# Kernel optimization log

Measured on AMD Instinct MI355X. Metric: run time of the kernel, lower is better.

Reference implementation:

```python
import jax, jax.numpy as jnp
import numpy as np

N = 50000      # nodes
E = 800000     # edges
F_IN = 146
D = 256        # repr_len
H = 512        # GENConv hidden (expansion=2)
L = 25         # res blocks
EPS_MSG = 1e-7 # GENConv message eps
T = 0.01       # softmax aggregation temperature


def setup_inputs() -> dict:
    key = jax.random.key(0)
    ks = jax.random.split(key, 8)
    s = lambda k, shape, scale=0.05: jax.random.normal(k, shape, jnp.float32) * scale
    return dict(
        x=jax.random.uniform(ks[0], (N, F_IN), jnp.float32),
        edge_index=jax.random.randint(ks[1], (2, E), 0, N, jnp.int32),
        enc_W=s(ks[2], (F_IN, D)), enc_b=jnp.zeros((D,), jnp.float32),
        conv_W1=s(ks[3], (L, D, H)), conv_b1=jnp.zeros((L, H), jnp.float32),
        conv_ln_g=jnp.ones((L, H), jnp.float32), conv_ln_b=jnp.zeros((L, H), jnp.float32),
        conv_W2=s(ks[4], (L, H, D)), conv_b2=jnp.zeros((L, D), jnp.float32),
        res_ln_g=jnp.ones((L, D), jnp.float32), res_ln_b=jnp.zeros((L, D), jnp.float32),
        fc1_W=s(ks[5], (D, D // 2)), fc1_b=jnp.zeros((D // 2,), jnp.float32),
        out_W=s(ks[6], (D // 2, 1)), out_b=jnp.zeros((1,), jnp.float32),
    )


def layer_norm(x, g, b, eps=1e-5):
    mu = x.mean(-1, keepdims=True)
    var = ((x - mu) ** 2).mean(-1, keepdims=True)
    return (x - mu) * jax.lax.rsqrt(var + eps) * g + b


def genconv(x, src, dst, W1, b1, g1, bb1, W2, b2):
    # message: relu(x_j) + eps  (no edge_attr)
    msg = jax.nn.relu(x[src]) + EPS_MSG                    # [E, D]
    logit = msg * T
    m = jax.ops.segment_max(logit, dst, num_segments=N)    # per-dst, per-feature max
    m = jnp.where(jnp.isfinite(m), m, 0.0)                 # isolated nodes -> 0
    num = jnp.exp(logit - m[dst])
    den = jax.ops.segment_sum(num, dst, num_segments=N)
    alpha = num / (den[dst] + 1e-16)
    agg = jax.ops.segment_sum(alpha * msg, dst, num_segments=N)  # [N, D]
    h = agg + x                                            # root residual inside GENConv
    h = jax.nn.relu(layer_norm(h @ W1 + b1, g1, bb1))      # MLP: Lin->LN->ReLU->Lin
    return h @ W2 + b2


def reference(x, edge_index, enc_W, enc_b, conv_W1, conv_b1, conv_ln_g, conv_ln_b,
              conv_W2, conv_b2, res_ln_g, res_ln_b, fc1_W, fc1_b, out_W, out_b):
    src, dst = edge_index[0], edge_index[1]
    x = x.at[:, 121:].set(x[:, 121:] / 100.0 - 0.5)
    h = x @ enc_W + enc_b
    # layer 0: conv only
    h = genconv(h, src, dst, conv_W1[0], conv_b1[0], conv_ln_g[0], conv_ln_b[0],
                conv_W2[0], conv_b2[0])

    # layers 1..24: res+ block  (dropout=0.1 is identity in eval mode)
    def step(h, p):
        W1, b1, g1, bb1, W2, b2, rg, rb = p
        z = jax.nn.relu(layer_norm(h, rg, rb))
        z = genconv(z, src, dst, W1, b1, g1, bb1, W2, b2)
        return h + z, None

    params = (conv_W1[1:], conv_b1[1:], conv_ln_g[1:], conv_ln_b[1:],
              conv_W2[1:], conv_b2[1:], res_ln_g[1:], res_ln_b[1:])
    h, _ = jax.lax.scan(step, h, params)

    # final: layers[0].act(layers[0].norm(x))
    h = jax.nn.relu(layer_norm(h, res_ln_g[0], res_ln_b[0]))
    h = jax.nn.relu(h @ fc1_W + fc1_b)
    return h @ out_W + out_b
```

## Files before the change

kernel.cpp:

```cpp
#include <hip/hip_runtime.h>

#define NN 50000
#define NE 800000
#define FIN 146
#define DD 256
#define HHD 512
#define NL 25
#define MT 196
#define MT2 391
#define SCAN_NB 49

#define SWZ(r) (((r) >> 1) & 3)

typedef _Float16 h8 __attribute__((ext_vector_type(8)));
typedef float f32x4 __attribute__((ext_vector_type(4)));
typedef unsigned short us8 __attribute__((ext_vector_type(8)));
typedef _Float16 hf4 __attribute__((ext_vector_type(4)));

__device__ __forceinline__ float wsum(float v) {
#pragma unroll
  for (int off = 32; off > 0; off >>= 1) v += __shfl_xor(v, off, 64);
  return v;
}

__device__ __forceinline__ unsigned short f16b(float x) {
  _Float16 h = (_Float16)x;
  return __builtin_bit_cast(unsigned short, h);
}
__device__ __forceinline__ float f16f(unsigned short b) {
  return (float)__builtin_bit_cast(_Float16, b);
}

__device__ __forceinline__ void gl_lds16(const void* g, void* l) {
  __builtin_amdgcn_global_load_lds(
      (const __attribute__((address_space(1))) unsigned int*)g,
      (__attribute__((address_space(3))) unsigned int*)l, 16, 0, 0);
}

__global__ void count_k(const int* __restrict__ ei, int* __restrict__ deg) {
  int e = blockIdx.x * 256 + threadIdx.x;
  if (e < NE) atomicAdd(&deg[ei[NE + e]], 1);
}

__global__ __launch_bounds__(1024) void scan1_k(const int* __restrict__ deg,
                                                int* __restrict__ rp,
                                                int* __restrict__ bsum) {
  __shared__ int buf[1024];
  int tid = threadIdx.x, blk = blockIdx.x;
  int i = blk * 1024 + tid;
  buf[tid] = (i < NN) ? deg[i] : 0;
  __syncthreads();
#pragma unroll
  for (int off = 1; off < 1024; off <<= 1) {
    int t = (tid >= off) ? buf[tid - off] : 0;
    __syncthreads();
    buf[tid] += t;
    __syncthreads();
  }
  if (i < NN) rp[i + 1] = buf[tid];
  if (tid == 1023) bsum[blk] = buf[1023];
}

__global__ void scan2_k(int* __restrict__ bsum) {
  int tid = threadIdx.x;
  int v = (tid < SCAN_NB) ? bsum[tid] : 0;
#pragma unroll
  for (int off = 1; off < 64; off <<= 1) {
    int t = __shfl_up(v, off, 64);
    if (tid >= off) v += t;
  }
  if (tid < SCAN_NB) bsum[tid] = v;
}

__global__ __launch_bounds__(1024) void scan3_k(const int* __restrict__ bsum,
                                                int* __restrict__ rp,
                                                int* __restrict__ deg) {
  int i = blockIdx.x * 1024 + threadIdx.x;
  if (i < NN) {
    int blk = i >> 10;
    if (blk > 0) rp[i + 1] += bsum[blk - 1];
    deg[i] = 0;
  }
  if (i == 0) rp[0] = 0;
}

__global__ void fill_k(const int* __restrict__ ei, const int* __restrict__ rp,
                       int* __restrict__ deg, int* __restrict__ col) {
  int e = blockIdx.x * 256 + threadIdx.x;
  if (e < NE) {
    int d = ei[NE + e];
    int pos = rp[d] + atomicAdd(&deg[d], 1);
    col[pos] = ei[e];
  }
}

__global__ __launch_bounds__(256) void wconv_k(const float* __restrict__ cW1,
                                               const float* __restrict__ cW2,
                                               const float* __restrict__ fcW,
                                               const float* __restrict__ encW,
                                               unsigned short* __restrict__ wbuf,
                                               unsigned short* __restrict__ fc1t,
                                               unsigned short* __restrict__ encT) {
  int z = blockIdx.z;
  const float* W;
  unsigned short* oh;
  int Ksrc, Kpad, N;
  if (z < 50) {
    int l = z >> 1, which = z & 1;
    if (which == 0) { W = cW1 + (size_t)l * 131072; Ksrc = 256; N = 512; oh = wbuf + (size_t)l * 524288; }
    else            { W = cW2 + (size_t)l * 131072; Ksrc = 512; N = 256; oh = wbuf + (size_t)l * 524288 + 262144; }
    Kpad = Ksrc;
  } else if (z == 50) {
    W = fcW; Ksrc = 256; Kpad = 256; N = 128; oh = fc1t;
  } else {
    W = encW; Ksrc = FIN; Kpad = 160; N = 256; oh = encT;
  }
  if ((int)blockIdx.x >= (Kpad >> 5) || (int)blockIdx.y >= (N >> 5)) return;
  __shared__ float tile[32][33];
  int tx = threadIdx.x, ty = threadIdx.y;
  int k0 = blockIdx.x * 32, n0 = blockIdx.y * 32;
#pragma unroll
  for (int i = 0; i < 4; ++i) {
    int r = ty + i * 8;
    int k = k0 + r;
    tile[r][tx] = (k < Ksrc) ? W[(size_t)k * N + n0 + tx] : 0.f;
  }
  __syncthreads();
#pragma unroll
  for (int i = 0; i < 4; ++i) {
    int r = ty + i * 8;
    float v = tile[tx][r];
    oh[(size_t)(n0 + r) * Kpad + k0 + tx] = f16b(v);
  }
}

__global__ __launch_bounds__(256) void agg16_k(const hf4* __restrict__ z16,
                                               const int* __restrict__ rp,
                                               const int* __restrict__ col,
                                               unsigned short* __restrict__ hh16) {
  int node = blockIdx.x * 4 + (threadIdx.x >> 6);
  int lane = threadIdx.x & 63;
  if (node >= NN) return;
  int beg = rp[node], end = rp[node + 1];
  float4 s = make_float4(0.f, 0.f, 0.f, 0.f);
  float4 v = make_float4(0.f, 0.f, 0.f, 0.f);
  int j = beg;
  for (; j + 1 < end; j += 2) {
    int sn0 = col[j], sn1 = col[j + 1];
    hf4 a = z16[(size_t)sn0 * 64 + lane];
    hf4 c = z16[(size_t)sn1 * 64 + lane];
    float m0 = fmaxf((float)a[0], 0.f) + 1e-7f;
    float m1 = fmaxf((float)a[1], 0.f) + 1e-7f;
    float m2 = fmaxf((float)a[2], 0.f) + 1e-7f;
    float m3 = fmaxf((float)a[3], 0.f) + 1e-7f;
    float e0 = __expf(m0 * 0.01f), e1 = __expf(m1 * 0.01f);
    float e2 = __expf(m2 * 0.01f), e3 = __expf(m3 * 0.01f);
    s.x += e0; s.y += e1; s.z += e2; s.w += e3;
    v.x = fmaf(e0, m0, v.x); v.y = fmaf(e1, m1, v.y);
    v.z = fmaf(e2, m2, v.z); v.w = fmaf(e3, m3, v.w);
    float n0 = fmaxf((float)c[0], 0.f) + 1e-7f;
    float n1 = fmaxf((float)c[1], 0.f) + 1e-7f;
    float n2 = fmaxf((float)c[2], 0.f) + 1e-7f;
    float n3 = fmaxf((float)c[3], 0.f) + 1e-7f;
    float f0 = __expf(n0 * 0.01f), f1 = __expf(n1 * 0.01f);
    float f2 = __expf(n2 * 0.01f), f3 = __expf(n3 * 0.01f);
    s.x += f0; s.y += f1; s.z += f2; s.w += f3;
    v.x = fmaf(f0, n0, v.x); v.y = fmaf(f1, n1, v.y);
    v.z = fmaf(f2, n2, v.z); v.w = fmaf(f3, n3, v.w);
  }
  if (j < end) {
    int sn = col[j];
    hf4 a = z16[(size_t)sn * 64 + lane];
    float m0 = fmaxf((float)a[0], 0.f) + 1e-7f;
    float m1 = fmaxf((float)a[1], 0.f) + 1e-7f;
    float m2 = fmaxf((float)a[2], 0.f) + 1e-7f;
    float m3 = fmaxf((float)a[3], 0.f) + 1e-7f;
    float e0 = __expf(m0 * 0.01f), e1 = __expf(m1 * 0.01f);
    float e2 = __expf(m2 * 0.01f), e3 = __expf(m3 * 0.01f);
    s.x += e0; s.y += e1; s.z += e2; s.w += e3;
    v.x = fmaf(e0, m0, v.x); v.y = fmaf(e1, m1, v.y);
    v.z = fmaf(e2, m2, v.z); v.w = fmaf(e3, m3, v.w);
  }
  hf4 ow = z16[(size_t)node * 64 + lane];
  float o0 = v.x / (s.x + 1e-16f) + (float)ow[0];
  float o1 = v.y / (s.y + 1e-16f) + (float)ow[1];
  float o2 = v.z / (s.z + 1e-16f) + (float)ow[2];
  float o3 = v.w / (s.w + 1e-16f) + (float)ow[3];
  size_t idx = (size_t)node * DD + lane * 4;
  *(ushort4*)&hh16[idx] = make_ushort4(f16b(o0), f16b(o1), f16b(o2), f16b(o3));
}

template <int AMODE, int ACC, int RELU, int PSUM, int C16, int Z16>
__global__ __launch_bounds__(512, 3) void mgemm_k(
    const float* __restrict__ Af, const unsigned short* __restrict__ A16,
    const unsigned short* __restrict__ BTh,
    const float* __restrict__ bias, float* __restrict__ C, int M, int K, int N,
    int mtiles, int lgnb,
    const float2* __restrict__ stats,
    const float* __restrict__ lng, const float* __restrict__ lnbeta,
    float2* __restrict__ psum_out, unsigned short* __restrict__ z16out) {
  __shared__ __align__(16) unsigned short Ash[2][8192], Bsh[2][4096];
  int tid = threadIdx.x;
  int bi = blockIdx.x;
  int ppx = (mtiles + 7) >> 3;
  int slot = bi >> 3;
  int panel = (bi & 7) * ppx + (slot >> lgnb);
  if (panel >= mtiles) return;
  int nblk = slot & ((1 << lgnb) - 1);
  int bm0 = panel * 256, bn0 = nblk * 128;
  int lane = tid & 63, wv = tid >> 6;
  int wr = (wv >> 1) * 64, wc = (wv & 1) * 64;
  int lr = lane & 15, lc = lane >> 4;
  f32x4 acc[4][4];
  f32x4 zf = {0.f, 0.f, 0.f, 0.f};
#pragma unroll
  for (int mi = 0; mi < 4; ++mi)
#pragma unroll
    for (int ni = 0; ni < 4; ++ni) acc[mi][ni] = zf;

  int sr = tid >> 1, hf = tid & 1;
  int arow = bm0 + sr;

  float mu = 0.f, rstd = 1.f;
  if constexpr (AMODE == 3) {
    if (arow < M) {
      float2 st = stats[arow];
      mu = st.x; rstd = st.y;
    }
  }

  auto stageB = [&](int buf, int k0) {
    int r = tid >> 2, cp = tid & 3;
    int c = cp ^ SWZ(r);
    gl_lds16(BTh + (size_t)(bn0 + r) * K + k0 + c * 8, &Bsh[buf][wv * 512]);
  };
  auto stageA = [&](int buf, int k0) {
    if constexpr (AMODE == 0) {
#pragma unroll
      for (int j = 0; j < 2; ++j) {
        int idx = wv * 128 + j * 64 + lane;
        int r = idx >> 2, cp = idx & 3;
        int c = cp ^ SWZ(r);
        int row = bm0 + r;
        if (row >= M) row = M - 1;
        gl_lds16(A16 + (size_t)row * K + k0 + c * 8, &Ash[buf][wv * 1024 + j * 512]);
      }
    } else {
      float v[16];
      if (arow < M) {
        if constexpr (AMODE == 2) {
          const float* xp = Af + (size_t)arow * FIN;
#pragma unroll
          for (int j = 0; j < 16; ++j) {
            int kk = k0 + hf * 16 + j;
            float t = (kk < FIN) ? xp[kk] : 0.f;
            if (kk >= 121 && kk < FIN) t = t * 0.01f - 0.5f;
            v[j] = t;
          }
        } else {
          const float* ap = Af + (size_t)arow * K + k0 + hf * 16;
          *(float4*)&v[0] = *(const float4*)(ap);
          *(float4*)&v[4] = *(const float4*)(ap + 4);
          *(float4*)&v[8] = *(const float4*)(ap + 8);
          *(float4*)&v[12] = *(const float4*)(ap + 12);
          const float* gp = lng + k0 + hf * 16;
          const float* bp = lnbeta + k0 + hf * 16;
#pragma unroll
          for (int j = 0; j < 16; ++j)
            v[j] = fmaxf(0.f, (v[j] - mu) * rstd * gp[j] + bp[j]);
        }
      } else {
#pragma unroll
        for (int j = 0; j < 16; ++j) v[j] = 0.f;
      }
      unsigned short hi[16];
#pragma unroll
      for (int j = 0; j < 16; ++j) hi[j] = f16b(v[j]);
      int c0 = hf * 2;
      *(us8*)&Ash[buf][sr * 32 + ((c0 ^ SWZ(sr)) * 8)] = *(us8*)&hi[0];
      *(us8*)&Ash[buf][sr * 32 + (((c0 + 1) ^ SWZ(sr)) * 8)] = *(us8*)&hi[8];
    }
  };

  int nt = K / 32;
  stageA(0, 0);
  stageB(0, 0);
  __syncthreads();
  for (int t = 0; t < nt; ++t) {
    int cur = t & 1;
    h8 a[4], bh[4];
#pragma unroll
    for (int mi = 0; mi < 4; ++mi) {
      int r = wr + mi * 16 + lr;
      a[mi] = *(const h8*)&Ash[cur][r * 32 + ((lc ^ SWZ(r)) * 8)];
    }
#pragma unroll
    for (int ni = 0; ni < 4; ++ni) {
      int n = wc + ni * 16 + lr;
      bh[ni] = *(const h8*)&Bsh[cur][n * 32 + ((lc ^ SWZ(n)) * 8)];
    }
    if (t + 1 < nt) {
      stageA(cur ^ 1, (t + 1) * 32);
      stageB(cur ^ 1, (t + 1) * 32);
    }
    __builtin_amdgcn_s_setprio(1);
#pragma unroll
    for (int mi = 0; mi < 4; ++mi)
#pragma unroll
      for (int ni = 0; ni < 4; ++ni)
        acc[mi][ni] = __builtin_amdgcn_mfma_f32_16x16x32_f16(a[mi], bh[ni], acc[mi][ni], 0, 0, 0);
    __builtin_amdgcn_s_setprio(0);
    __syncthreads();
  }
  float sloc[16], qloc[16];
  if constexpr (PSUM) {
#pragma unroll
    for (int i = 0; i < 16; ++i) { sloc[i] = 0.f; qloc[i] = 0.f; }
  }
#pragma unroll
  for (int ni = 0; ni < 4; ++ni) {
    int colg = bn0 + wc + ni * 16 + lr;
    float bia = bias[colg];
#pragma unroll
    for (int mi = 0; mi < 4; ++mi) {
#pragma unroll
      for (int r = 0; r < 4; ++r) {
        int row = bm0 + wr + mi * 16 + lc * 4 + r;
        if (row < M) {
          float vv = acc[mi][ni][r] + bia;
          if (ACC) vv += C[(size_t)row * N + colg];
          if (RELU) vv = fmaxf(vv, 0.f);
          if constexpr (C16) {
            ((unsigned short*)C)[(size_t)row * N + colg] = f16b(vv);
          } else {
            C[(size_t)row * N + colg] = vv;
          }
          if constexpr (Z16) {
            z16out[(size_t)row * N + colg] = f16b(vv);
          }
          if constexpr (PSUM) {
            sloc[mi * 4 + r] += vv;
            qloc[mi * 4 + r] = fmaf(vv, vv, qloc[mi * 4 + r]);
          }
        }
      }
    }
  }
  if constexpr (PSUM) {
#pragma unroll
    for (int i = 0; i < 16; ++i) {
      float s = sloc[i], q = qloc[i];
#pragma unroll
      for (int off = 1; off < 16; off <<= 1) {
        s += __shfl_xor(s, off, 64);
        q += __shfl_xor(q, off, 64);
      }
      sloc[i] = s; qloc[i] = q;
    }
    __syncthreads();
    float2* lps = (float2*)&Ash[0][0];
    if (wv & 1) {
      if (lr == 0) {
#pragma unroll
        for (int mi = 0; mi < 4; ++mi)
#pragma unroll
          for (int r = 0; r < 4; ++r)
            lps[(wv >> 1) * 64 + mi * 16 + lc * 4 + r] =
                make_float2(sloc[mi * 4 + r], qloc[mi * 4 + r]);
      }
    }
    __syncthreads();
    if (!(wv & 1)) {
      if (lr == 0) {
#pragma unroll
        for (int mi = 0; mi < 4; ++mi)
#pragma unroll
          for (int r = 0; r < 4; ++r) {
            int rl = mi * 16 + lc * 4 + r;
            float2 o = lps[(wv >> 1) * 64 + rl];
            int row = bm0 + wr + rl;
            if (row < M)
              psum_out[(size_t)row * 4 + nblk] =
                  make_float2(sloc[mi * 4 + r] + o.x, qloc[mi * 4 + r] + o.y);
          }
      }
    }
  }
}

template <int ACC, int LAST>
__global__ __launch_bounds__(512, 3) void mgemm2_k(
    const unsigned short* __restrict__ A16,
    const unsigned short* __restrict__ BTh,
    const float* __restrict__ bias, float* __restrict__ C,
    const float2* __restrict__ psum_in,
    const float* __restrict__ lng, const float* __restrict__ lnbeta,
    const float* __restrict__ rg, const float* __restrict__ rb,
    unsigned short* __restrict__ z16o, float2* __restrict__ hstats) {
  __shared__ __align__(16) unsigned short Ash[2][4096], Bsh[2][8192];
  const int M = NN, K = HHD, N = DD;
  int tid = threadIdx.x;
  int bi = blockIdx.x;
  int panel = (bi & 7) * 49 + (bi >> 3);
  if (panel >= MT2) return;
  int bm0 = panel * 128;
  int lane = tid & 63, wv = tid >> 6;
  int wr = (wv >> 2) * 64, wc = (wv & 3) * 64;
  int lr = lane & 15, lc = lane >> 4;
  f32x4 acc[4][4];
  f32x4 zf = {0.f, 0.f, 0.f, 0.f};
#pragma unroll
  for (int mi = 0; mi < 4; ++mi)
#pragma unroll
    for (int ni = 0; ni < 4; ++ni) acc[mi][ni] = zf;

  int sr2 = tid >> 2, q = tid & 3;
  int arow = bm0 + sr2;
  float mu = 0.f, rstd = 1.f;
  if (arow < M) {
    float2 p0 = psum_in[(size_t)arow * 4 + 0];
    float2 p1 = psum_in[(size_t)arow * 4 + 1];
    float2 p2 = psum_in[(size_t)arow * 4 + 2];
    float2 p3 = psum_in[(size_t)arow * 4 + 3];
    float s = p0.x + p1.x + p2.x + p3.x;
    float qq = p0.y + p1.y + p2.y + p3.y;
    mu = s * (1.0f / HHD);
    float var = qq * (1.0f / HHD) - mu * mu;
    rstd = rsqrtf(var + 1e-5f);
  }

  auto stageB = [&](int buf, int k0) {
#pragma unroll
    for (int j = 0; j < 2; ++j) {
      int idx = j * 512 + tid;
      int r = idx >> 2, cp = idx & 3;
      int c = cp ^ SWZ(r);
      gl_lds16(BTh + (size_t)r * K + k0 + c * 8, &Bsh[buf][(j * 512 + wv * 64) * 8]);
    }
  };
  auto stageA = [&](int buf, int k0) {
    float v[8];
    if (arow < M) {
      us8 p0 = *(const us8*)(A16 + (size_t)arow * K + k0 + q * 8);
      const float* gp = lng + k0 + q * 8;
      const float* bp = lnbeta + k0 + q * 8;
#pragma unroll
      for (int j = 0; j < 8; ++j)
        v[j] = fmaxf(0.f, (f16f(p0[j]) - mu) * rstd * gp[j] + bp[j]);
    } else {
#pragma unroll
      for (int j = 0; j < 8; ++j) v[j] = 0.f;
    }
    unsigned short hi[8];
#pragma unroll
    for (int j = 0; j < 8; ++j) hi[j] = f16b(v[j]);
    *(us8*)&Ash[buf][sr2 * 32 + ((q ^ SWZ(sr2)) * 8)] = *(us8*)&hi[0];
  };

  const int nt = HHD / 32;
  stageA(0, 0);
  stageB(0, 0);
  __syncthreads();
  for (int t = 0; t < nt; ++t) {
    int cur = t & 1;
    h8 a[4], bh[4];
#pragma unroll
    for (int mi = 0; mi < 4; ++mi) {
      int r = wr + mi * 16 + lr;
      a[mi] = *(const h8*)&Ash[cur][r * 32 + ((lc ^ SWZ(r)) * 8)];
    }
#pragma unroll
    for (int ni = 0; ni < 4; ++ni) {
      int n = wc + ni * 16 + lr;
      bh[ni] = *(const h8*)&Bsh[cur][n * 32 + ((lc ^ SWZ(n)) * 8)];
    }
    if (t + 1 < nt) {
      stageA(cur ^ 1, (t + 1) * 32);
      stageB(cur ^ 1, (t + 1) * 32);
    }
    __builtin_amdgcn_s_setprio(1);
#pragma unroll
    for (int mi = 0; mi < 4; ++mi)
#pragma unroll
      for (int ni = 0; ni < 4; ++ni)
        acc[mi][ni] = __builtin_amdgcn_mfma_f32_16x16x32_f16(a[mi], bh[ni], acc[mi][ni], 0, 0, 0);
    __builtin_amdgcn_s_setprio(0);
    __syncthreads();
  }
  float sloc[16], qloc[16];
#pragma unroll
  for (int i = 0; i < 16; ++i) { sloc[i] = 0.f; qloc[i] = 0.f; }
#pragma unroll
  for (int ni = 0; ni < 4; ++ni) {
    int colg = wc + ni * 16 + lr;
    float bia = bias[colg];
#pragma unroll
    for (int mi = 0; mi < 4; ++mi) {
#pragma unroll
      for (int r = 0; r < 4; ++r) {
        int row = bm0 + wr + mi * 16 + lc * 4 + r;
        float vv = acc[mi][ni][r] + bia;
        if (row < M) {
          if (ACC) vv += C[(size_t)row * N + colg];
          C[(size_t)row * N + colg] = vv;
        }
        acc[mi][ni][r] = vv;
        sloc[mi * 4 + r] += vv;
        qloc[mi * 4 + r] = fmaf(vv, vv, qloc[mi * 4 + r]);
      }
    }
  }
#pragma unroll
  for (int i = 0; i < 16; ++i) {
    float s = sloc[i], qq = qloc[i];
#pragma unroll
    for (int off = 1; off < 16; off <<= 1) {
      s += __shfl_xor(s, off, 64);
      qq += __shfl_xor(qq, off, 64);
    }
    sloc[i] = s; qloc[i] = qq;
  }
  __syncthreads();
  float2* lpart = (float2*)&Bsh[0][0];
  float2* rowst = (float2*)&Bsh[1][0];
  if (lr == 0) {
#pragma unroll
    for (int mi = 0; mi < 4; ++mi)
#pragma unroll
      for (int r = 0; r < 4; ++r) {
        int rl = wr + mi * 16 + lc * 4 + r;
        lpart[rl * 4 + (wv & 3)] = make_float2(sloc[mi * 4 + r], qloc[mi * 4 + r]);
      }
  }
  __syncthreads();
  if (tid < 128) {
    float2 p0 = lpart[tid * 4 + 0];
    float2 p1 = lpart[tid * 4 + 1];
    float2 p2 = lpart[tid * 4 + 2];
    float2 p3 = lpart[tid * 4 + 3];
    float s = p0.x + p1.x + p2.x + p3.x;
    float qq = p0.y + p1.y + p2.y + p3.y;
    float m_ = s * (1.0f / DD);
    float var = qq * (1.0f / DD) - m_ * m_;
    float rs = rsqrtf(var + 1e-5f);
    rowst[tid] = make_float2(m_, rs);
    if (LAST) {
      int row = bm0 + tid;
      if (row < M) hstats[row] = make_float2(m_, rs);
    }
  }
  __syncthreads();
  if (!LAST) {
#pragma unroll
    for (int mi = 0; mi < 4; ++mi) {
#pragma unroll
      for (int r = 0; r < 4; ++r) {
        int rl = wr + mi * 16 + lc * 4 + r;
        int row = bm0 + rl;
        if (row < M) {
          float2 st = rowst[rl];
#pragma unroll
          for (int ni = 0; ni < 4; ++ni) {
            int colg = wc + ni * 16 + lr;
            float z = fmaxf(0.f, (acc[mi][ni][r] - st.x) * st.y * rg[colg] + rb[colg]);
            z16o[(size_t)row * N + colg] = f16b(z);
          }
        }
      }
    }
  }
}

__global__ __launch_bounds__(256) void outmv_k(const float* __restrict__ t1,
                                               const float* __restrict__ oW,
                                               const float* __restrict__ ob,
                                               float* __restrict__ out) {
  int row = blockIdx.x * 4 + (threadIdx.x >> 6);
  int lane = threadIdx.x & 63;
  if (row >= NN) return;
  float2 v = *(const float2*)(t1 + (size_t)row * 128 + lane * 2);
  float2 w = *(const float2*)(oW + lane * 2);
  float s = v.x * w.x + v.y * w.y;
  s = wsum(s);
  if (lane == 0) out[row] = s + ob[0];
}

extern "C" void kernel_launch(void* const* d_in, const int* in_sizes, int n_in,
                              void* d_out, int out_size, void* d_ws, size_t ws_size,
                              hipStream_t stream) {
  const float* x = (const float*)d_in[0];
  const int* ei = (const int*)d_in[1];
  const float* encW = (const float*)d_in[2];
  const float* encb = (const float*)d_in[3];
  const float* cW1 = (const float*)d_in[4];
  const float* cb1 = (const float*)d_in[5];
  const float* clg = (const float*)d_in[6];
  const float* clb = (const float*)d_in[7];
  const float* cW2 = (const float*)d_in[8];
  const float* cb2 = (const float*)d_in[9];
  const float* rlg = (const float*)d_in[10];
  const float* rlb = (const float*)d_in[11];
  const float* fcW = (const float*)d_in[12];
  const float* fcb = (const float*)d_in[13];
  const float* oW = (const float*)d_in[14];
  const float* ob = (const float*)d_in[15];
  float* out = (float*)d_out;

  char* w = (char*)d_ws;
  float* h = (float*)(w);
  unsigned short* mid16 = (unsigned short*)(w + 51200000);
  float* t1 = (float*)(w + 51200000);
  hf4* z16 = (hf4*)(w + 102400000);
  unsigned short* hh16 = (unsigned short*)(w + 128000000);
  float2* psum = (float2*)(w + 153600000);
  float2* hstats = (float2*)(w + 155200000);
  int* rp = (int*)(w + 155600000);
  int* deg = (int*)(w + 155800064);
  int* col = (int*)(w + 156000128);
  unsigned short* wbuf = (unsigned short*)(w + 159200128);
  unsigned short* fc1t = (unsigned short*)(w + 185414528);
  unsigned short* encT = (unsigned short*)(w + 185545600);
  int* bsum = (int*)(w + 185709664);

  hipMemsetAsync(deg, 0, NN * sizeof(int), stream);
  count_k<<<(NE + 255) / 256, 256, 0, stream>>>(ei, deg);
  scan1_k<<<SCAN_NB, 1024, 0, stream>>>(deg, rp, bsum);
  scan2_k<<<1, 64, 0, stream>>>(bsum);
  scan3_k<<<SCAN_NB, 1024, 0, stream>>>(bsum, rp, deg);
  fill_k<<<(NE + 255) / 256, 256, 0, stream>>>(ei, rp, deg, col);

  wconv_k<<<dim3(16, 16, 52), dim3(32, 8), 0, stream>>>(cW1, cW2, fcW, encW, wbuf, fc1t, encT);

  mgemm_k<2, 0, 0, 0, 0, 1><<<400, 512, 0, stream>>>(
      x, nullptr, encT, encb, h, NN, 160, DD, MT, 1,
      nullptr, nullptr, nullptr, nullptr, (unsigned short*)z16);

  for (int l = 0; l < NL; ++l) {
    agg16_k<<<NN / 4, 256, 0, stream>>>(z16, rp, col, hh16);

    const unsigned short* w1h = wbuf + (size_t)l * 524288;
    mgemm_k<0, 0, 0, 1, 1, 0><<<800, 512, 0, stream>>>(
        nullptr, hh16, w1h, cb1 + (size_t)l * HHD, (float*)mid16,
        NN, DD, HHD, MT, 2, nullptr, nullptr, nullptr, psum, nullptr);

    const unsigned short* w2h = wbuf + (size_t)l * 524288 + 262144;
    const float* lg = clg + (size_t)l * HHD;
    const float* lb = clb + (size_t)l * HHD;
    if (l == 0) {
      mgemm2_k<0, 0><<<392, 512, 0, stream>>>(
          mid16, w2h, cb2 + (size_t)l * DD, h, psum, lg, lb,
          rlg + (size_t)(l + 1) * DD, rlb + (size_t)(l + 1) * DD,
          (unsigned short*)z16, nullptr);
    } else if (l < NL - 1) {
      mgemm2_k<1, 0><<<392, 512, 0, stream>>>(
          mid16, w2h, cb2 + (size_t)l * DD, h, psum, lg, lb,
          rlg + (size_t)(l + 1) * DD, rlb + (size_t)(l + 1) * DD,
          (unsigned short*)z16, nullptr);
    } else {
      mgemm2_k<1, 1><<<392, 512, 0, stream>>>(
          mid16, w2h, cb2 + (size_t)l * DD, h, psum, lg, lb,
          rlg, rlb, (unsigned short*)z16, hstats);
    }
  }

  mgemm_k<3, 0, 1, 0, 0, 0><<<200, 512, 0, stream>>>(
      h, nullptr, fc1t, fcb, t1, NN, DD, 128, MT, 0,
      hstats, rlg, rlb, nullptr, nullptr);
  outmv_k<<<NN / 4, 256, 0, stream>>>(t1, oW, ob, out);
}
```

Measured before the change: 5.084 ms.

## Store residual stream in fp16 and unroll edge aggregation by four

Switches the residual hidden state h from fp32 to fp16 storage. The second GEMM reads and writes it as half precision, the encoder writes fp16 directly, and layer 0 aggregation reads that buffer in place of a separate z16 copy. The final fc1 GEMM now loads the fp16 h. This halves the bytes of the residual read-modify-write in every layer. The edge aggregation loop is also unrolled to four neighbours to issue more gathers at once. The risk is accumulated rounding error from keeping the residual sum in fp16 across 25 layers.

Result: faster. 4.740 ms (-6.8%).

```diff
diff --git a/kernel.cpp b/kernel.cpp
--- a/kernel.cpp
+++ b/kernel.cpp
@@ -145,30 +145,27 @@
   float4 s = make_float4(0.f, 0.f, 0.f, 0.f);
   float4 v = make_float4(0.f, 0.f, 0.f, 0.f);
   int j = beg;
-  for (; j + 1 < end; j += 2) {
-    int sn0 = col[j], sn1 = col[j + 1];
-    hf4 a = z16[(size_t)sn0 * 64 + lane];
-    hf4 c = z16[(size_t)sn1 * 64 + lane];
-    float m0 = fmaxf((float)a[0], 0.f) + 1e-7f;
-    float m1 = fmaxf((float)a[1], 0.f) + 1e-7f;
-    float m2 = fmaxf((float)a[2], 0.f) + 1e-7f;
-    float m3 = fmaxf((float)a[3], 0.f) + 1e-7f;
-    float e0 = __expf(m0 * 0.01f), e1 = __expf(m1 * 0.01f);
-    float e2 = __expf(m2 * 0.01f), e3 = __expf(m3 * 0.01f);
-    s.x += e0; s.y += e1; s.z += e2; s.w += e3;
-    v.x = fmaf(e0, m0, v.x); v.y = fmaf(e1, m1, v.y);
-    v.z = fmaf(e2, m2, v.z); v.w = fmaf(e3, m3, v.w);
-    float n0 = fmaxf((float)c[0], 0.f) + 1e-7f;
-    float n1 = fmaxf((float)c[1], 0.f) + 1e-7f;
-    float n2 = fmaxf((float)c[2], 0.f) + 1e-7f;
-    float n3 = fmaxf((float)c[3], 0.f) + 1e-7f;
-    float f0 = __expf(n0 * 0.01f), f1 = __expf(n1 * 0.01f);
-    float f2 = __expf(n2 * 0.01f), f3 = __expf(n3 * 0.01f);
-    s.x += f0; s.y += f1; s.z += f2; s.w += f3;
-    v.x = fmaf(f0, n0, v.x); v.y = fmaf(f1, n1, v.y);
-    v.z = fmaf(f2, n2, v.z); v.w = fmaf(f3, n3, v.w);
-  }
-  if (j < end) {
+  for (; j + 3 < end; j += 4) {
+    int sn0 = col[j], sn1 = col[j + 1], sn2 = col[j + 2], sn3 = col[j + 3];
+    hf4 a0 = z16[(size_t)sn0 * 64 + lane];
+    hf4 a1 = z16[(size_t)sn1 * 64 + lane];
+    hf4 a2 = z16[(size_t)sn2 * 64 + lane];
+    hf4 a3 = z16[(size_t)sn3 * 64 + lane];
+#pragma unroll
+    for (int u = 0; u < 4; ++u) {
+      hf4 a = (u == 0) ? a0 : (u == 1) ? a1 : (u == 2) ? a2 : a3;
+      float m0 = fmaxf((float)a[0], 0.f) + 1e-7f;
+      float m1 = fmaxf((float)a[1], 0.f) + 1e-7f;
+      float m2 = fmaxf((float)a[2], 0.f) + 1e-7f;
+      float m3 = fmaxf((float)a[3], 0.f) + 1e-7f;
+      float e0 = __expf(m0 * 0.01f), e1 = __expf(m1 * 0.01f);
+      float e2 = __expf(m2 * 0.01f), e3 = __expf(m3 * 0.01f);
+      s.x += e0; s.y += e1; s.z += e2; s.w += e3;
+      v.x = fmaf(e0, m0, v.x); v.y = fmaf(e1, m1, v.y);
+      v.z = fmaf(e2, m2, v.z); v.w = fmaf(e3, m3, v.w);
+    }
+  }
+  for (; j < end; ++j) {
     int sn = col[j];
     hf4 a = z16[(size_t)sn * 64 + lane];
     float m0 = fmaxf((float)a[0], 0.f) + 1e-7f;
@@ -258,16 +255,16 @@
             v[j] = t;
           }
         } else {
-          const float* ap = Af + (size_t)arow * K + k0 + hf * 16;
-          *(float4*)&v[0] = *(const float4*)(ap);
-          *(float4*)&v[4] = *(const float4*)(ap + 4);
-          *(float4*)&v[8] = *(const float4*)(ap + 8);
-          *(float4*)&v[12] = *(const float4*)(ap + 12);
+          const unsigned short* ap = A16 + (size_t)arow * K + k0 + hf * 16;
+          us8 p0 = *(const us8*)(ap);
+          us8 p1 = *(const us8*)(ap + 8);
           const float* gp = lng + k0 + hf * 16;
           const float* bp = lnbeta + k0 + hf * 16;
 #pragma unroll
-          for (int j = 0; j < 16; ++j)
-            v[j] = fmaxf(0.f, (v[j] - mu) * rstd * gp[j] + bp[j]);
+          for (int j = 0; j < 8; ++j) {
+            v[j] = fmaxf(0.f, (f16f(p0[j]) - mu) * rstd * gp[j] + bp[j]);
+            v[8 + j] = fmaxf(0.f, (f16f(p1[j]) - mu) * rstd * gp[8 + j] + bp[8 + j]);
+          }
         }
       } else {
 #pragma unroll
@@ -392,7 +389,7 @@
 __global__ __launch_bounds__(512, 3) void mgemm2_k(
     const unsigned short* __restrict__ A16,
     const unsigned short* __restrict__ BTh,
-    const float* __restrict__ bias, float* __restrict__ C,
+    const float* __restrict__ bias, unsigned short* __restrict__ h16,
     const float2* __restrict__ psum_in,
     const float* __restrict__ lng, const float* __restrict__ lnbeta,
     const float* __restrict__ rg, const float* __restrict__ rb,
@@ -501,8 +498,8 @@
         int row = bm0 + wr + mi * 16 + lc * 4 + r;
         float vv = acc[mi][ni][r] + bia;
         if (row < M) {
-          if (ACC) vv += C[(size_t)row * N + colg];
-          C[(size_t)row * N + colg] = vv;
+          if (ACC) vv += f16f(h16[(size_t)row * N + colg]);
+          h16[(size_t)row * N + colg] = f16b(vv);
         }
         acc[mi][ni][r] = vv;
         sloc[mi * 4 + r] += vv;
@@ -607,7 +604,7 @@
   float* out = (float*)d_out;
 
   char* w = (char*)d_ws;
-  float* h = (float*)(w);
+  unsigned short* h16 = (unsigned short*)(w);
   unsigned short* mid16 = (unsigned short*)(w + 51200000);
   float* t1 = (float*)(w + 51200000);
   hf4* z16 = (hf4*)(w + 102400000);
@@ -631,12 +628,13 @@
 
   wconv_k<<<dim3(16, 16, 52), dim3(32, 8), 0, stream>>>(cW1, cW2, fcW, encW, wbuf, fc1t, encT);
 
-  mgemm_k<2, 0, 0, 0, 0, 1><<<400, 512, 0, stream>>>(
-      x, nullptr, encT, encb, h, NN, 160, DD, MT, 1,
-      nullptr, nullptr, nullptr, nullptr, (unsigned short*)z16);
+  mgemm_k<2, 0, 0, 0, 1, 0><<<400, 512, 0, stream>>>(
+      x, nullptr, encT, encb, (float*)h16, NN, 160, DD, MT, 1,
+      nullptr, nullptr, nullptr, nullptr, nullptr);
 
   for (int l = 0; l < NL; ++l) {
-    agg16_k<<<NN / 4, 256, 0, stream>>>(z16, rp, col, hh16);
+    const hf4* zsrc = (l == 0) ? (const hf4*)h16 : z16;
+    agg16_k<<<NN / 4, 256, 0, stream>>>(zsrc, rp, col, hh16);
 
     const unsigned short* w1h = wbuf + (size_t)l * 524288;
     mgemm_k<0, 0, 0, 1, 1, 0><<<800, 512, 0, stream>>>(
@@ -648,23 +646,23 @@
     const float* lb = clb + (size_t)l * HHD;
     if (l == 0) {
       mgemm2_k<0, 0><<<392, 512, 0, stream>>>(
-          mid16, w2h, cb2 + (size_t)l * DD, h, psum, lg, lb,
+          mid16, w2h, cb2 + (size_t)l * DD, h16, psum, lg, lb,
           rlg + (size_t)(l + 1) * DD, rlb + (size_t)(l + 1) * DD,
           (unsigned short*)z16, nullptr);
     } else if (l < NL - 1) {
       mgemm2_k<1, 0><<<392, 512, 0, stream>>>(
-          mid16, w2h, cb2 + (size_t)l * DD, h, psum, lg, lb,
+          mid16, w2h, cb2 + (size_t)l * DD, h16, psum, lg, lb,
           rlg + (size_t)(l + 1) * DD, rlb + (size_t)(l + 1) * DD,
           (unsigned short*)z16, nullptr);
     } else {
       mgemm2_k<1, 1><<<392, 512, 0, stream>>>(
-          mid16, w2h, cb2 + (size_t)l * DD, h, psum, lg, lb,
+          mid16, w2h, cb2 + (size_t)l * DD, h16, psum, lg, lb,
           rlg, rlb, (unsigned short*)z16, hstats);
     }
   }
 
   mgemm_k<3, 0, 1, 0, 0, 0><<<200, 512, 0, stream>>>(
-      h, nullptr, fc1t, fcb, t1, NN, DD, 128, MT, 0,
+      nullptr, h16, fc1t, fcb, t1, NN, DD, 128, MT, 0,
       hstats, rlg, rlb, nullptr, nullptr);
   outmv_k<<<NN / 4, 256, 0, stream>>>(t1, oW, ob, out);
 }
```
